# Kernel optimization log

Measured on AMD Instinct MI355X. Metric: run time of the kernel, lower is better.

## Reference

```python
import jax, jax.numpy as jnp
import numpy as np
from jax.ops import segment_sum

N = 50000        # nodes
E = 800000       # edges
IN = 128         # in_channels
HID = 128        # hidden_channels
G = 256          # number of graphs


def setup_inputs() -> dict:
    key = jax.random.key(0)
    ks = jax.random.split(key, 24)

    def w(k, shape, fan_in):
        return (jax.random.normal(k, shape, dtype=jnp.float32) / np.sqrt(fan_in)).astype(jnp.float32)

    x = jax.random.normal(ks[0], (N, IN), dtype=jnp.float32)
    pos = jax.random.normal(ks[1], (N, 3), dtype=jnp.float32)
    edge_index = jax.random.randint(ks[2], (2, E), 0, N, dtype=jnp.int64)
    batch = jnp.sort(jax.random.randint(ks[3], (N,), 0, G, dtype=jnp.int64))

    params = dict(
        gcn_w=w(ks[4], (IN, HID), IN), gcn_b=jnp.zeros((HID,), jnp.float32),
        pam_w=w(ks[5], (IN, HID), IN), pam_b=jnp.zeros((HID,), jnp.float32),
        pm_w1=w(ks[6], (3, HID), 3), pm_b1=jnp.zeros((HID,), jnp.float32),
        pm_w2=w(ks[7], (HID, HID), HID), pm_b2=jnp.zeros((HID,), jnp.float32),
        att_w=w(ks[8], (2 * HID, 1), 2 * HID), att_b=jnp.zeros((1,), jnp.float32),
        fus_w=w(ks[9], (2 * HID, HID), 2 * HID), fus_b=jnp.zeros((HID,), jnp.float32),
        l1_w=w(ks[10], (HID, HID // 2), HID), l1_b=jnp.zeros((HID // 2,), jnp.float32),
        l2_w=w(ks[11], (HID // 2, 1), HID // 2), l2_b=jnp.zeros((1,), jnp.float32),
    )
    return dict(x=x, pos=pos, edge_index=edge_index, batch=batch, **params)


def reference(x, pos, edge_index, batch,
              gcn_w, gcn_b, pam_w, pam_b,
              pm_w1, pm_b1, pm_w2, pm_b2,
              att_w, att_b, fus_w, fus_b,
              l1_w, l1_b, l2_w, l2_b):
    n = x.shape[0]
    src, dst = edge_index[0], edge_index[1]  # j = source, i = target (PyG flow)

    # ---- global branch: GCNConv (self-loops + symmetric normalization) ----
    xw = x @ gcn_w                                   # [N, HID]
    loop = jnp.arange(n, dtype=src.dtype)
    s = jnp.concatenate([src, loop])
    d = jnp.concatenate([dst, loop])
    deg = segment_sum(jnp.ones_like(d, dtype=xw.dtype), d, num_segments=n)
    dinv = jnp.where(deg > 0, deg ** -0.5, 0.0)
    norm = dinv[s] * dinv[d]                          # [E+N]
    gcn = segment_sum(norm[:, None] * xw[s], d, num_segments=n) + gcn_b
    global_feat = jax.nn.relu(gcn)

    # ---- local branch: PAMConv ----
    xl = x @ pam_w + pam_b                            # [N, HID]
    x_i, x_j = xl[dst], xl[src]                       # [E, HID]
    delta = pos[dst] - pos[src]                       # [E, 3]
    de = jax.nn.relu(delta @ pm_w1 + pm_b1) @ pm_w2 + pm_b2   # [E, HID]
    att = jax.nn.sigmoid(jnp.concatenate([x_i, x_j], axis=-1) @ att_w + att_b)  # [E,1]
    msg = att * (x_j + de)
    local_feat = jax.nn.relu(segment_sum(msg, dst, num_segments=n))

    # ---- fusion + global mean pool + readout ----
    fused = jax.nn.relu(jnp.concatenate([global_feat, local_feat], axis=-1) @ fus_w + fus_b)
    counts = segment_sum(jnp.ones((n,), fused.dtype), batch, num_segments=G)
    pooled = segment_sum(fused, batch, num_segments=G) / jnp.clip(counts, 1.0)[:, None]
    h = jax.nn.relu(pooled @ l1_w + l1_b)
    return h @ l2_w + l2_b                            # [G, 1]
```

## Files before the change

kernel.cpp:

```cpp
#include <hip/hip_runtime.h>
#include <math.h>

#define NN 50000
#define NE 800000
#define HD 128
#define NG 256
#define SCAN_B 196
#define NODE_B 12500
#define AGG_B 25000
#define HIST_B 3125
#define GEM_B 782
#define ZQ2 8192
#define WP_HIST0 73

typedef unsigned int u32;
typedef unsigned short u16;
typedef __attribute__((ext_vector_type(8))) short bf16x8;
typedef __attribute__((ext_vector_type(4))) float f32x4;
typedef __attribute__((ext_vector_type(2))) float f32x2;

__device__ __forceinline__ float wave_allsum(float v) {
#pragma unroll
  for (int m = 1; m < 64; m <<= 1) v += __shfl_xor(v, m, 64);
  return v;
}
__device__ __forceinline__ float bcastf(float v, int t) {
  return __int_as_float(__builtin_amdgcn_readlane(__float_as_int(v), t));
}
__device__ __forceinline__ u32 f2b_bits(float f) {
  u32 u = __float_as_uint(f);
  return (u + 0x7fffu + ((u >> 16) & 1u)) >> 16;
}
__device__ __forceinline__ u32 cvtpk_bf16(float lo, float hi) {
  u32 r;
  asm("v_cvt_pk_bf16_f32 %0, %1, %2" : "=v"(r) : "v"(lo), "v"(hi));
  return r;
}
__device__ __forceinline__ f32x2 splat2(float v) { return (f32x2){v, v}; }
__device__ __forceinline__ f32x2 pkfma(f32x2 a, f32x2 b, f32x2 c) {
  return a * b + c;
}

__global__ __launch_bounds__(256) void k_wpack(
    const float* __restrict__ gcn_w, const float* __restrict__ pam_w,
    const float* __restrict__ pm_w2, const float* __restrict__ fus_w,
    const float* __restrict__ pam_b, const float* __restrict__ att_w,
    const float* __restrict__ att_b, const float* __restrict__ pm_b2,
    u16* __restrict__ Bg, u16* __restrict__ Bl, u16* __restrict__ Bf,
    float* __restrict__ vi, float* __restrict__ vj,
    float* __restrict__ consts, float* __restrict__ bsumv,
    uint4* __restrict__ zr2, const int* __restrict__ ei,
    int* __restrict__ cnt, u16* __restrict__ slot16) {
  if (blockIdx.x >= WP_HIST0) {
    const int e = (blockIdx.x - WP_HIST0) * 256 + threadIdx.x;
    if (e < NE) slot16[e] = (u16)atomicAdd(&cnt[ei[NE + e]], 1);
    return;
  }
  if (blockIdx.x >= 41) {
    const int zi = (blockIdx.x - 41) * 256 + threadIdx.x;
    if (zi < ZQ2) zr2[zi] = (uint4){0u, 0u, 0u, 0u};
    return;
  }
  if (blockIdx.x == 40) {
    const int t = threadIdx.x;
    const int k = t & 127;
    const float* w = att_w + (t >> 7) * HD;
    float s = 0.f;
    for (int h = 0; h < HD; ++h) s = fmaf(pam_w[k * HD + h], w[h], s);
    if (t < 128) {
      vi[k] = s;
      bsumv[k] = pam_b[k] + pm_b2[k];
    } else {
      vj[k] = s;
    }
    if (t < 64) {
      float p = fmaf(pam_b[t], att_w[t], pam_b[t + 64] * att_w[t + 64]);
      p = wave_allsum(p);
      if (t == 0) consts[0] = p + att_b[0];
    } else if (t < 128) {
      const int l = t - 64;
      float p =
          fmaf(pam_b[l], att_w[HD + l], pam_b[l + 64] * att_w[HD + 64 + l]);
      p = wave_allsum(p);
      if (l == 0) consts[1] = p;
    }
    return;
  }
  const int t = blockIdx.x * 256 + threadIdx.x;
  const float* W;
  u16* dst;
  if (t < 2048) {
    const int kb = t >> 7, n = t & 127;
    W = gcn_w + (size_t)kb * 8 * HD + n;
    dst = Bg + (size_t)t * 8;
  } else if (t < 6144) {
    const int u = t - 2048;
    const int kb = u >> 7, n = u & 127;
    W = ((kb < 16) ? (pam_w + (size_t)kb * 8 * HD)
                   : (pm_w2 + (size_t)(kb - 16) * 8 * HD)) +
        n;
    dst = Bl + (size_t)u * 8;
  } else {
    const int u = t - 6144;
    const int kb = u >> 7, n = u & 127;
    W = fus_w + (size_t)kb * 8 * HD + n;
    dst = Bf + (size_t)u * 8;
  }
  union {
    u16 o[8];
    uint4 v;
  } pk;
#pragma unroll
  for (int i = 0; i < 8; ++i) pk.o[i] = (u16)f2b_bits(W[i * HD]);
  *(uint4*)dst = pk.v;
}

__global__ __launch_bounds__(256) void k_scan1(const int* __restrict__ cnt,
                                               int* __restrict__ bsum) {
  const int i = blockIdx.x * 256 + threadIdx.x;
  int v = (i < NN) ? cnt[i] : 0;
#pragma unroll
  for (int m = 1; m < 64; m <<= 1) v += __shfl_xor(v, m, 64);
  __shared__ int s[4];
  if ((threadIdx.x & 63) == 0) s[threadIdx.x >> 6] = v;
  __syncthreads();
  if (threadIdx.x == 0) bsum[blockIdx.x] = s[0] + s[1] + s[2] + s[3];
}

__global__ __launch_bounds__(256) void k_scan23(
    const int* __restrict__ cnt, const int* __restrict__ bsum,
    const float* __restrict__ pos, int* __restrict__ offs,
    float* __restrict__ dinv, float4* __restrict__ pos4) {
  __shared__ int s[256];
  const int t = threadIdx.x;
  const int bv = (t < SCAN_B) ? bsum[t] : 0;
  s[t] = bv;
  __syncthreads();
  for (int d = 1; d < 256; d <<= 1) {
    int add = (t >= d) ? s[t - d] : 0;
    __syncthreads();
    s[t] += add;
    __syncthreads();
  }
  const int bpre = (blockIdx.x > 0) ? s[blockIdx.x - 1] : 0;
  __syncthreads();
  const int i = blockIdx.x * 256 + t;
  const int v = (i < NN) ? cnt[i] : 0;
  s[t] = v;
  __syncthreads();
  for (int d = 1; d < 256; d <<= 1) {
    int add = (t >= d) ? s[t - d] : 0;
    __syncthreads();
    s[t] += add;
    __syncthreads();
  }
  if (i < NN) {
    offs[i] = bpre + s[t] - v;
    dinv[i] = __builtin_amdgcn_rsqf((float)v + 1.0f);
    pos4[i] = make_float4(pos[3 * i], pos[3 * i + 1], pos[3 * i + 2], 0.f);
  }
}

__global__ __launch_bounds__(256) void k_scatgc(
    const int* __restrict__ ei, const int* __restrict__ offs,
    const u16* __restrict__ slot16, int* __restrict__ csr_src,
    const int* __restrict__ batch, float* __restrict__ counts,
    const float* __restrict__ x, const float* __restrict__ dinv,
    const int* __restrict__ cnt, const float* __restrict__ vi,
    const float* __restrict__ vj, const float* __restrict__ consts,
    u16* __restrict__ xq, float* __restrict__ ai_arr,
    float2* __restrict__ adj2) {
  if (blockIdx.x < HIST_B) {
    const int e = blockIdx.x * 256 + threadIdx.x;
    if (e < NE) {
      const int d = ei[NE + e];
      csr_src[offs[d] + slot16[e]] = ei[e];
    }
    return;
  }
  if (blockIdx.x == HIST_B) {
    const int g = threadIdx.x;
    int lo = 0, hi = NN;
    while (lo < hi) {
      const int mid = (lo + hi) >> 1;
      if (batch[mid] < g) lo = mid + 1; else hi = mid;
    }
    const int b0 = lo;
    hi = NN;
    while (lo < hi) {
      const int mid = (lo + hi) >> 1;
      if (batch[mid] <= g) lo = mid + 1; else hi = mid;
    }
    counts[g] = (float)(lo - b0);
    return;
  }
  const int wave = threadIdx.x >> 6, lane = threadIdx.x & 63;
  const int i = (blockIdx.x - HIST_B - 1) * 4 + wave;
  if (i >= NN) return;
  const float2 v = *(const float2*)&x[(size_t)i * HD + lane * 2];
  const float dv = dinv[i];
  const u32 q = __builtin_amdgcn_cvt_pk_fp8_f32(dv * v.x, dv * v.y, 0u, false);
  xq[(size_t)i * 64 + lane] = (u16)q;
  const float2 a = *(const float2*)&vi[lane * 2];
  const float2 b = *(const float2*)&vj[lane * 2];
  float si = wave_allsum(fmaf(v.x, a.x, v.y * a.y));
  float sj = wave_allsum(fmaf(v.x, b.x, v.y * b.y));
  if (lane == 0) {
    ai_arr[i] = si + consts[0];
    adj2[i] = make_float2(sj + consts[1], sqrtf((float)cnt[i] + 1.0f));
  }
}

__global__ __launch_bounds__(256) void k_agg(
    const u16* __restrict__ xq, const float4* __restrict__ pos4,
    const float2* __restrict__ adj2, const int* __restrict__ csr_src,
    const int* __restrict__ offs, const int* __restrict__ cnt,
    const float* __restrict__ ai_arr, const float* __restrict__ pm_w1,
    const float* __restrict__ pm_b1, u32* __restrict__ ZG,
    u32* __restrict__ XT, float* __restrict__ sa_out) {
  __shared__ float part[2][64][9];
  const int w = threadIdx.x >> 6, lane = threadIdx.x & 63;
  const int nl = w >> 1, half = w & 1;
  const int i = blockIdx.x * 2 + nl;
  const int c0 = lane * 2;

  const f32x2 w1x = *(const f32x2*)&pm_w1[c0];
  const f32x2 w1y = *(const f32x2*)&pm_w1[HD + c0];
  const f32x2 w1z = *(const f32x2*)&pm_w1[2 * HD + c0];
  const f32x2 b1 = *(const f32x2*)&pm_b1[c0];
  const float ai = ai_arr[i];
  const float4 pi = pos4[i];

  f32x2 zg = {0.f, 0.f}, xa = {0.f, 0.f}, tt = {0.f, 0.f};
  float sa = 0.f;
  const int b = offs[i], c = cnt[i];
  const int hf = (c + 1) >> 1;
  const int lo = b + (half ? hf : 0);
  const int hiE = half ? (b + c) : (b + hf);
  for (int base = lo; base < hiE; base += 64) {
    const int mm = min(64, hiE - base);
    const int sk = csr_src[base + ((lane < mm) ? lane : 0)];
    const float2 a2 = adj2[sk];
    float attk = __builtin_amdgcn_rcpf(1.f + __expf(-(ai + a2.x)));
    const float4 ps = pos4[sk];
    const float apk = attk * a2.y;
    const float dxk = pi.x - ps.x;
    const float dyk = pi.y - ps.y;
    const float dzk = pi.z - ps.z;
    if (lane >= mm) attk = 0.f;
    sa += wave_allsum(attk);

    for (int s16 = 0; s16 < mm; s16 += 16) {
      const int n16 = min(16, mm - s16);
      u32 rr[16];
#pragma unroll
      for (int u = 0; u < 16; ++u) {
        if (u < n16) {
          const int s = __builtin_amdgcn_readlane(sk, s16 + u);
          rr[u] = *(xq + ((size_t)s << 6) + lane);
        }
      }
#pragma unroll
      for (int u = 0; u < 16; ++u) {
        if (u < n16) {
          const int T = s16 + u;
          const float att = bcastf(attk, T);
          const float ap = bcastf(apk, T);
          const float dx = bcastf(dxk, T);
          const float dy = bcastf(dyk, T);
          const float dz = bcastf(dzk, T);
          const f32x2 y = __builtin_amdgcn_cvt_pk_f32_fp8(rr[u], false);
          zg += y;
          xa = pkfma(splat2(ap), y, xa);
          f32x2 gg = pkfma(splat2(dz), w1z,
                           pkfma(splat2(dy), w1y,
                                 pkfma(splat2(dx), w1x, b1)));
          gg = __builtin_elementwise_max(gg, splat2(0.f));
          tt = pkfma(splat2(att), gg, tt);
        }
      }
    }
  }
  if (half) {
    float* p = part[nl][lane];
    p[0] = zg.x; p[1] = zg.y;
    p[2] = xa.x; p[3] = xa.y;
    p[4] = tt.x; p[5] = tt.y;
    p[6] = sa;
  }
  __syncthreads();
  if (!half) {
    const float* p = part[nl][lane];
    zg.x += p[0]; zg.y += p[1];
    xa.x += p[2]; xa.y += p[3];
    tt.x += p[4]; tt.y += p[5];
    sa += p[6];
    const u32 xi = *(xq + ((size_t)i << 6) + lane);
    zg += __builtin_amdgcn_cvt_pk_f32_fp8(xi, false);
    ZG[(size_t)i * 64 + lane] = cvtpk_bf16(zg.x, zg.y);
    XT[(size_t)i * 128 + lane] = cvtpk_bf16(xa.x, xa.y);
    XT[(size_t)i * 128 + 64 + lane] = cvtpk_bf16(tt.x, tt.y);
    if (lane == 0) sa_out[i] = sa;
  }
}

template <int K16>
__device__ __forceinline__ void phase_g(const u16* __restrict__ pa,
                                        const u16* __restrict__ pb0,
                                        f32x4 acc[8]) {
  bf16x8 a[2], b[2][8];
  a[0] = *(const bf16x8*)pa;
#pragma unroll
  for (int cf = 0; cf < 8; ++cf) b[0][cf] = *(const bf16x8*)(pb0 + cf * 128);
#pragma unroll
  for (int k0 = 0; k0 < K16; ++k0) {
    if (k0 + 1 < K16) {
      a[(k0 + 1) & 1] = *(const bf16x8*)(pa + (k0 + 1) * 32);
      const u16* pn = pb0 + (size_t)(k0 + 1) * 4096;
#pragma unroll
      for (int cf = 0; cf < 8; ++cf)
        b[(k0 + 1) & 1][cf] = *(const bf16x8*)(pn + cf * 128);
    }
#pragma unroll
    for (int cf = 0; cf < 8; ++cf)
      acc[cf] = __builtin_amdgcn_mfma_f32_16x16x32_bf16(
          a[k0 & 1], b[k0 & 1][cf], acc[cf], 0, 0, 0);
  }
}

__global__ __launch_bounds__(256, 3) void k_gemms(
    const u16* __restrict__ ZG, const u16* __restrict__ XT,
    const u16* __restrict__ Bg, const u16* __restrict__ Bl,
    const u16* __restrict__ Bf, const float* __restrict__ dinv,
    const float* __restrict__ sa, const float* __restrict__ gcn_b,
    const float* __restrict__ bsumv, const float* __restrict__ fus_b,
    const int* __restrict__ batch, float* __restrict__ pooled) {
  __shared__ u16 T[64 * 256];
  __shared__ int batch_lds[64];
  const int n0 = blockIdx.x * 64;
  const int t = threadIdx.x, lane = t & 63, w = t >> 6;
  const int m = lane & 15, g = lane >> 4;
  const int r0 = w * 16;

  if (t < 64) batch_lds[t] = (n0 + t < NN) ? batch[n0 + t] : -1;

  float dv[4], sv[4];
#pragma unroll
  for (int j = 0; j < 4; ++j) {
    const int rr = min(n0 + r0 + g * 4 + j, NN - 1);
    dv[j] = dinv[rr];
    sv[j] = sa[rr];
  }
  float bgv[8], bsv[8];
#pragma unroll
  for (int cf = 0; cf < 8; ++cf) {
    bgv[cf] = gcn_b[cf * 16 + m];
    bsv[cf] = bsumv[cf * 16 + m];
  }

  const int rowA = min(n0 + r0 + m, NN - 1);
  f32x4 acc[8];

#pragma unroll
  for (int cf = 0; cf < 8; ++cf) acc[cf] = (f32x4){0.f, 0.f, 0.f, 0.f};
  phase_g<4>(ZG + (size_t)rowA * 128 + g * 8, Bg + ((size_t)g * HD + m) * 8,
             acc);
#pragma unroll
  for (int j = 0; j < 4; ++j) {
    const int rl = r0 + g * 4 + j;
#pragma unroll
    for (int cf = 0; cf < 8; ++cf) {
      const float v = fmaxf(fmaf(dv[j], acc[cf][j], bgv[cf]), 0.f);
      T[rl * 256 + ((cf * 16 + m) ^ ((rl & 7) << 3))] = (u16)f2b_bits(v);
    }
  }

#pragma unroll
  for (int cf = 0; cf < 8; ++cf) acc[cf] = (f32x4){0.f, 0.f, 0.f, 0.f};
  phase_g<8>(XT + (size_t)rowA * 256 + g * 8, Bl + ((size_t)g * HD + m) * 8,
             acc);
#pragma unroll
  for (int j = 0; j < 4; ++j) {
    const int rl = r0 + g * 4 + j;
#pragma unroll
    for (int cf = 0; cf < 8; ++cf) {
      const float v = fmaxf(fmaf(sv[j], bsv[cf], acc[cf][j]), 0.f);
      T[rl * 256 + ((128 + cf * 16 + m) ^ ((rl & 7) << 3))] = (u16)f2b_bits(v);
    }
  }

  const int x0m = (m & 7) << 3;
  const u16* rowT = &T[(r0 + m) * 256];
  const u16* pbC = Bf + ((size_t)g * HD + m) * 8;
#pragma unroll
  for (int cf = 0; cf < 8; ++cf) acc[cf] = (f32x4){0.f, 0.f, 0.f, 0.f};
  {
    bf16x8 a[2], b[2][8];
    a[0] = *(const bf16x8*)&rowT[(g * 8) ^ x0m];
#pragma unroll
    for (int cf = 0; cf < 8; ++cf) b[0][cf] = *(const bf16x8*)(pbC + cf * 128);
#pragma unroll
    for (int k0 = 0; k0 < 8; ++k0) {
      if (k0 + 1 < 8) {
        a[(k0 + 1) & 1] = *(const bf16x8*)&rowT[(g * 8 + (k0 + 1) * 32) ^ x0m];
        const u16* pn = pbC + (size_t)(k0 + 1) * 4096;
#pragma unroll
        for (int cf = 0; cf < 8; ++cf)
          b[(k0 + 1) & 1][cf] = *(const bf16x8*)(pn + cf * 128);
      }
#pragma unroll
      for (int cf = 0; cf < 8; ++cf)
        acc[cf] = __builtin_amdgcn_mfma_f32_16x16x32_bf16(
            a[k0 & 1], b[k0 & 1][cf], acc[cf], 0, 0, 0);
    }
  }
  float* F = (float*)T;
#pragma unroll
  for (int j = 0; j < 4; ++j) {
    const int rl = r0 + g * 4 + j;
#pragma unroll
    for (int cf = 0; cf < 8; ++cf)
      F[rl * 128 + ((cf * 16 + m) ^ ((rl & 12) << 2))] =
          fmaxf(acc[cf][j] + fus_b[cf * 16 + m], 0.f);
  }
  __syncthreads();

  const int col = t & 127;
  const int q = t >> 7;
  int seg = -1;
  float run = 0.f;
  for (int r = q * 32; r < q * 32 + 32; ++r) {
    const int bg = batch_lds[r];
    const float v = F[r * 128 + (col ^ ((r & 12) << 2))];
    if (bg != seg) {
      if (seg >= 0) atomicAdd(&pooled[seg * HD + col], run);
      seg = bg;
      run = 0.f;
    }
    if (bg >= 0) run += v;
  }
  if (seg >= 0) atomicAdd(&pooled[seg * HD + col], run);
}

__global__ __launch_bounds__(64) void k_head(const float* __restrict__ pooled,
                                             const float* __restrict__ counts,
                                             const float* __restrict__ l1w,
                                             const float* __restrict__ l1b,
                                             const float* __restrict__ l2w,
                                             const float* __restrict__ l2b,
                                             float* __restrict__ out) {
  const int g = blockIdx.x, j = threadIdx.x;
  const float inv = __builtin_amdgcn_rcpf(fmaxf(counts[g], 1.f));
  float acc = l1b[j];
  for (int k = 0; k < HD; ++k)
    acc = fmaf(pooled[g * HD + k] * inv, l1w[k * 64 + j], acc);
  float v = fmaxf(acc, 0.f) * l2w[j];
  v = wave_allsum(v);
  if (j == 0) out[g] = v + l2b[0];
}

extern "C" void kernel_launch(void* const* d_in, const int* in_sizes, int n_in,
                              void* d_out, int out_size, void* d_ws,
                              size_t ws_size, hipStream_t stream) {
  const float* x = (const float*)d_in[0];
  const float* pos = (const float*)d_in[1];
  const int* ei = (const int*)d_in[2];
  const int* batch = (const int*)d_in[3];
  const float* gcn_w = (const float*)d_in[4];
  const float* gcn_b = (const float*)d_in[5];
  const float* pam_w = (const float*)d_in[6];
  const float* pam_b = (const float*)d_in[7];
  const float* pm_w1 = (const float*)d_in[8];
  const float* pm_b1 = (const float*)d_in[9];
  const float* pm_w2 = (const float*)d_in[10];
  const float* pm_b2 = (const float*)d_in[11];
  const float* att_w = (const float*)d_in[12];
  const float* att_b = (const float*)d_in[13];
  const float* fus_w = (const float*)d_in[14];
  const float* fus_b = (const float*)d_in[15];
  const float* l1_w = (const float*)d_in[16];
  const float* l1_b = (const float*)d_in[17];
  const float* l2_w = (const float*)d_in[18];
  const float* l2_b = (const float*)d_in[19];
  float* out = (float*)d_out;

  size_t off = 0;
  auto alloc = [&](size_t bytes) {
    void* p = (char*)d_ws + off;
    off += (bytes + 255) & ~size_t(255);
    return p;
  };
  u16* xq = (u16*)alloc((size_t)NN * 64 * 2);
  u32* ZG = (u32*)alloc((size_t)NN * 64 * 4);
  u32* XT = (u32*)alloc((size_t)NN * 128 * 4);
  float* sa = (float*)alloc((size_t)NN * 4);
  float* ai = (float*)alloc((size_t)NN * 4);
  float* dinv = (float*)alloc((size_t)NN * 4);
  float2* adj2 = (float2*)alloc((size_t)NN * 8);
  float4* pos4 = (float4*)alloc((size_t)NN * 16);
  float* pooled = (float*)alloc((size_t)NG * HD * 4);
  float* counts = (float*)alloc((size_t)NG * 4);
  int* cnt = (int*)alloc((size_t)NN * 4);
  int* offs = (int*)alloc((size_t)NN * 4);
  int* csr_src = (int*)alloc((size_t)NE * 4);
  u16* slot16 = (u16*)alloc((size_t)NE * 2);
  int* bsum = (int*)alloc((size_t)SCAN_B * 4);
  u16* Bg = (u16*)alloc((size_t)16 * 128 * 8 * 2);
  u16* Bl = (u16*)alloc((size_t)32 * 128 * 8 * 2);
  u16* Bf = (u16*)alloc((size_t)32 * 128 * 8 * 2);
  float* vi = (float*)alloc(128 * 4);
  float* vj = (float*)alloc(128 * 4);
  float* consts = (float*)alloc(2 * 4);
  float* bsumv = (float*)alloc(128 * 4);

  hipMemsetAsync(cnt, 0, NN * 4, stream);
  k_wpack<<<WP_HIST0 + HIST_B, 256, 0, stream>>>(
      gcn_w, pam_w, pm_w2, fus_w, pam_b, att_w, att_b, pm_b2, Bg, Bl, Bf, vi,
      vj, consts, bsumv, (uint4*)pooled, ei, cnt, slot16);
  k_scan1<<<SCAN_B, 256, 0, stream>>>(cnt, bsum);
  k_scan23<<<SCAN_B, 256, 0, stream>>>(cnt, bsum, pos, offs, dinv, pos4);
  k_scatgc<<<HIST_B + 1 + NODE_B, 256, 0, stream>>>(
      ei, offs, slot16, csr_src, batch, counts, x, dinv, cnt, vi, vj, consts,
      xq, ai, adj2);
  k_agg<<<AGG_B, 256, 0, stream>>>(xq, pos4, adj2, csr_src, offs, cnt, ai,
                                   pm_w1, pm_b1, ZG, XT, sa);
  k_gemms<<<GEM_B, 256, 0, stream>>>((const u16*)ZG, (const u16*)XT, Bg, Bl,
                                     Bf, dinv, sa, gcn_b, bsumv, fus_b, batch,
                                     pooled);
  k_head<<<NG, 64, 0, stream>>>(pooled, counts, l1_w, l1_b, l2_w, l2_b, out);
}
```

Before: 170.1 us.

## Pack attention/degree into pos4 padding and use one wave per node in aggregation

The per-node attention term and sqrt-degree are stored as two fp16 values in the unused w slot of the position float4, so each edge does one gather instead of two. The aggregation kernel now gives each node a single wave instead of splitting its edges across two waves with an LDS reduction and block sync. The inner loop becomes branch-free: the first 16 source rows are fetched before the attention math, and padded lanes are neutralised with zero weights. This adds fp16 rounding of the attention logit and degree, and it does wasted work on partial 16-edge groups.

Result: slower. 178.3 us (+4.8%).

```diff
diff --git a/kernel.cpp b/kernel.cpp
--- a/kernel.cpp
+++ b/kernel.cpp
@@ -1,4 +1,5 @@
 #include <hip/hip_runtime.h>
+#include <hip/hip_fp16.h>
 #include <math.h>
 
 #define NN 50000
@@ -7,7 +8,6 @@
 #define NG 256
 #define SCAN_B 196
 #define NODE_B 12500
-#define AGG_B 25000
 #define HIST_B 3125
 #define GEM_B 782
 #define ZQ2 8192
@@ -130,7 +130,7 @@
 __global__ __launch_bounds__(256) void k_scan23(
     const int* __restrict__ cnt, const int* __restrict__ bsum,
     const float* __restrict__ pos, int* __restrict__ offs,
-    float* __restrict__ dinv, float4* __restrict__ pos4) {
+    float* __restrict__ dinv, float4* __restrict__ posadj) {
   __shared__ int s[256];
   const int t = threadIdx.x;
   const int bv = (t < SCAN_B) ? bsum[t] : 0;
@@ -157,7 +157,7 @@
   if (i < NN) {
     offs[i] = bpre + s[t] - v;
     dinv[i] = __builtin_amdgcn_rsqf((float)v + 1.0f);
-    pos4[i] = make_float4(pos[3 * i], pos[3 * i + 1], pos[3 * i + 2], 0.f);
+    posadj[i] = make_float4(pos[3 * i], pos[3 * i + 1], pos[3 * i + 2], 0.f);
   }
 }
 
@@ -169,7 +169,7 @@
     const int* __restrict__ cnt, const float* __restrict__ vi,
     const float* __restrict__ vj, const float* __restrict__ consts,
     u16* __restrict__ xq, float* __restrict__ ai_arr,
-    float2* __restrict__ adj2) {
+    float4* __restrict__ posadj) {
   if (blockIdx.x < HIST_B) {
     const int e = blockIdx.x * 256 + threadIdx.x;
     if (e < NE) {
@@ -207,21 +207,23 @@
   float sj = wave_allsum(fmaf(v.x, b.x, v.y * b.y));
   if (lane == 0) {
     ai_arr[i] = si + consts[0];
-    adj2[i] = make_float2(sj + consts[1], sqrtf((float)cnt[i] + 1.0f));
-  }
-}
-
-__global__ __launch_bounds__(256) void k_agg(
-    const u16* __restrict__ xq, const float4* __restrict__ pos4,
-    const float2* __restrict__ adj2, const int* __restrict__ csr_src,
-    const int* __restrict__ offs, const int* __restrict__ cnt,
-    const float* __restrict__ ai_arr, const float* __restrict__ pm_w1,
-    const float* __restrict__ pm_b1, u32* __restrict__ ZG,
-    u32* __restrict__ XT, float* __restrict__ sa_out) {
-  __shared__ float part[2][64][9];
-  const int w = threadIdx.x >> 6, lane = threadIdx.x & 63;
-  const int nl = w >> 1, half = w & 1;
-  const int i = blockIdx.x * 2 + nl;
+    const u32 wb =
+        (u32)__half_as_ushort(__float2half(sj + consts[1])) |
+        ((u32)__half_as_ushort(__float2half(sqrtf((float)cnt[i] + 1.f)))
+         << 16);
+    ((float*)(posadj + i))[3] = __uint_as_float(wb);
+  }
+}
+
+__global__ __launch_bounds__(256, 4) void k_agg(
+    const u16* __restrict__ xq, const float4* __restrict__ posadj,
+    const int* __restrict__ csr_src, const int* __restrict__ offs,
+    const int* __restrict__ cnt, const float* __restrict__ ai_arr,
+    const float* __restrict__ pm_w1, const float* __restrict__ pm_b1,
+    u32* __restrict__ ZG, u32* __restrict__ XT, float* __restrict__ sa_out) {
+  const int wave = threadIdx.x >> 6, lane = threadIdx.x & 63;
+  const int i = blockIdx.x * 4 + wave;
+  if (i >= NN) return;
   const int c0 = lane * 2;
 
   const f32x2 w1x = *(const f32x2*)&pm_w1[c0];
@@ -229,79 +231,65 @@
   const f32x2 w1z = *(const f32x2*)&pm_w1[2 * HD + c0];
   const f32x2 b1 = *(const f32x2*)&pm_b1[c0];
   const float ai = ai_arr[i];
-  const float4 pi = pos4[i];
+  const float4 pi = posadj[i];
 
   f32x2 zg = {0.f, 0.f}, xa = {0.f, 0.f}, tt = {0.f, 0.f};
   float sa = 0.f;
-  const int b = offs[i], c = cnt[i];
-  const int hf = (c + 1) >> 1;
-  const int lo = b + (half ? hf : 0);
-  const int hiE = half ? (b + c) : (b + hf);
-  for (int base = lo; base < hiE; base += 64) {
-    const int mm = min(64, hiE - base);
+  const int b = offs[i], e = b + cnt[i];
+  for (int base = b; base < e; base += 64) {
+    const int mm = min(64, e - base);
     const int sk = csr_src[base + ((lane < mm) ? lane : 0)];
-    const float2 a2 = adj2[sk];
-    float attk = __builtin_amdgcn_rcpf(1.f + __expf(-(ai + a2.x)));
-    const float4 ps = pos4[sk];
-    const float apk = attk * a2.y;
-    const float dxk = pi.x - ps.x;
-    const float dyk = pi.y - ps.y;
-    const float dzk = pi.z - ps.z;
-    if (lane >= mm) attk = 0.f;
+    u32 rr[16];
+#pragma unroll
+    for (int u = 0; u < 16; ++u)
+      rr[u] = xq[((size_t)__builtin_amdgcn_readlane(sk, u) << 6) + lane];
+    const float4 pa = posadj[sk];
+    const u32 wb = __float_as_uint(pa.w);
+    const float aj = __half2float(__ushort_as_half((u16)(wb & 0xffffu)));
+    const float sdeg = __half2float(__ushort_as_half((u16)(wb >> 16)));
+    float attk = __builtin_amdgcn_rcpf(1.f + __expf(-(ai + aj)));
+    float onek = 1.f;
+    if (lane >= mm) { attk = 0.f; onek = 0.f; }
+    const float apk = attk * sdeg;
+    const float dxk = pi.x - pa.x;
+    const float dyk = pi.y - pa.y;
+    const float dzk = pi.z - pa.z;
     sa += wave_allsum(attk);
 
     for (int s16 = 0; s16 < mm; s16 += 16) {
-      const int n16 = min(16, mm - s16);
-      u32 rr[16];
+      if (s16) {
+#pragma unroll
+        for (int u = 0; u < 16; ++u)
+          rr[u] = xq[((size_t)__builtin_amdgcn_readlane(sk, (s16 + u) & 63)
+                      << 6) +
+                     lane];
+      }
 #pragma unroll
       for (int u = 0; u < 16; ++u) {
-        if (u < n16) {
-          const int s = __builtin_amdgcn_readlane(sk, s16 + u);
-          rr[u] = *(xq + ((size_t)s << 6) + lane);
-        }
+        const int T = (s16 + u) & 63;
+        const float att = bcastf(attk, T);
+        const float ap = bcastf(apk, T);
+        const float one = bcastf(onek, T);
+        const float dx = bcastf(dxk, T);
+        const float dy = bcastf(dyk, T);
+        const float dz = bcastf(dzk, T);
+        const f32x2 y = __builtin_amdgcn_cvt_pk_f32_fp8(rr[u], false);
+        zg = pkfma(splat2(one), y, zg);
+        xa = pkfma(splat2(ap), y, xa);
+        f32x2 gg = pkfma(splat2(dz), w1z,
+                         pkfma(splat2(dy), w1y, pkfma(splat2(dx), w1x, b1)));
+        gg = __builtin_elementwise_max(gg, splat2(0.f));
+        tt = pkfma(splat2(att), gg, tt);
       }
-#pragma unroll
-      for (int u = 0; u < 16; ++u) {
-        if (u < n16) {
-          const int T = s16 + u;
-          const float att = bcastf(attk, T);
-          const float ap = bcastf(apk, T);
-          const float dx = bcastf(dxk, T);
-          const float dy = bcastf(dyk, T);
-          const float dz = bcastf(dzk, T);
-          const f32x2 y = __builtin_amdgcn_cvt_pk_f32_fp8(rr[u], false);
-          zg += y;
-          xa = pkfma(splat2(ap), y, xa);
-          f32x2 gg = pkfma(splat2(dz), w1z,
-                           pkfma(splat2(dy), w1y,
-                                 pkfma(splat2(dx), w1x, b1)));
-          gg = __builtin_elementwise_max(gg, splat2(0.f));
-          tt = pkfma(splat2(att), gg, tt);
-        }
-      }
-    }
-  }
-  if (half) {
-    float* p = part[nl][lane];
-    p[0] = zg.x; p[1] = zg.y;
-    p[2] = xa.x; p[3] = xa.y;
-    p[4] = tt.x; p[5] = tt.y;
-    p[6] = sa;
-  }
-  __syncthreads();
-  if (!half) {
-    const float* p = part[nl][lane];
-    zg.x += p[0]; zg.y += p[1];
-    xa.x += p[2]; xa.y += p[3];
-    tt.x += p[4]; tt.y += p[5];
-    sa += p[6];
-    const u32 xi = *(xq + ((size_t)i << 6) + lane);
-    zg += __builtin_amdgcn_cvt_pk_f32_fp8(xi, false);
-    ZG[(size_t)i * 64 + lane] = cvtpk_bf16(zg.x, zg.y);
-    XT[(size_t)i * 128 + lane] = cvtpk_bf16(xa.x, xa.y);
-    XT[(size_t)i * 128 + 64 + lane] = cvtpk_bf16(tt.x, tt.y);
-    if (lane == 0) sa_out[i] = sa;
-  }
+    }
+  }
+  const u32 xi = xq[((size_t)i << 6) + lane];
+  zg += __builtin_amdgcn_cvt_pk_f32_fp8(xi, false);
+
+  ZG[(size_t)i * 64 + lane] = cvtpk_bf16(zg.x, zg.y);
+  XT[(size_t)i * 128 + lane] = cvtpk_bf16(xa.x, xa.y);
+  XT[(size_t)i * 128 + 64 + lane] = cvtpk_bf16(tt.x, tt.y);
+  if (lane == 0) sa_out[i] = sa;
 }
 
 template <int K16>
@@ -496,8 +484,7 @@
   float* sa = (float*)alloc((size_t)NN * 4);
   float* ai = (float*)alloc((size_t)NN * 4);
   float* dinv = (float*)alloc((size_t)NN * 4);
-  float2* adj2 = (float2*)alloc((size_t)NN * 8);
-  float4* pos4 = (float4*)alloc((size_t)NN * 16);
+  float4* posadj = (float4*)alloc((size_t)NN * 16);
   float* pooled = (float*)alloc((size_t)NG * HD * 4);
   float* counts = (float*)alloc((size_t)NG * 4);
   int* cnt = (int*)alloc((size_t)NN * 4);
@@ -518,12 +505,12 @@
       gcn_w, pam_w, pm_w2, fus_w, pam_b, att_w, att_b, pm_b2, Bg, Bl, Bf, vi,
       vj, consts, bsumv, (uint4*)pooled, ei, cnt, slot16);
   k_scan1<<<SCAN_B, 256, 0, stream>>>(cnt, bsum);
-  k_scan23<<<SCAN_B, 256, 0, stream>>>(cnt, bsum, pos, offs, dinv, pos4);
+  k_scan23<<<SCAN_B, 256, 0, stream>>>(cnt, bsum, pos, offs, dinv, posadj);
   k_scatgc<<<HIST_B + 1 + NODE_B, 256, 0, stream>>>(
       ei, offs, slot16, csr_src, batch, counts, x, dinv, cnt, vi, vj, consts,
-      xq, ai, adj2);
-  k_agg<<<AGG_B, 256, 0, stream>>>(xq, pos4, adj2, csr_src, offs, cnt, ai,
-                                   pm_w1, pm_b1, ZG, XT, sa);
+      xq, ai, posadj);
+  k_agg<<<NODE_B, 256, 0, stream>>>(xq, posadj, csr_src, offs, cnt, ai, pm_w1,
+                                    pm_b1, ZG, XT, sa);
   k_gemms<<<GEM_B, 256, 0, stream>>>((const u16*)ZG, (const u16*)XT, Bg, Bl,
                                      Bf, dinv, sa, gcn_b, bsumv, fus_b, batch,
                                      pooled);
```
